# Performance work log

Measured on AMD Instinct MI355X. Metric: run time of the kernel, lower is better.

Reference implementation:

```python
import jax, jax.numpy as jnp
import numpy as np

B, L, N, D = 16, 4096, 512, 256
EPS = 1e-8  # torch F.cosine_similarity default eps


def setup_inputs() -> dict:
    key = jax.random.key(0)
    k1, k2, k3 = jax.random.split(key, 3)
    spk_decoder_out = jax.random.normal(k1, (B, L, D), dtype=jnp.float32)
    profile = jax.random.normal(k2, (B, N, D), dtype=jnp.float32)
    # lengths in [1, N] so every batch has at least one valid profile
    profile_lens = jax.random.randint(k3, (B,), 1, N + 1, dtype=jnp.int32)
    return {"spk_decoder_out": spk_decoder_out, "profile": profile,
            "profile_lens": profile_lens}


def reference(spk_decoder_out, profile, profile_lens):
    # cosine similarity between (B,L,1,D) and (B,1,N,D) along D, computed
    # without materializing the (B,L,N,D) broadcast intermediate
    dots = jnp.einsum('bld,bnd->bln', spk_decoder_out, profile)      # (B,L,N)
    x_norm = jnp.sqrt(jnp.sum(spk_decoder_out * spk_decoder_out, axis=-1))  # (B,L)
    p_norm = jnp.sqrt(jnp.sum(profile * profile, axis=-1))           # (B,N)
    denom = jnp.maximum(x_norm[:, :, None] * p_norm[:, None, :], EPS)
    sim = dots / denom                                               # (B,L,N)

    # pad mask over profiles: True where n >= profile_lens[b]
    n = profile.shape[1]
    mask = jnp.arange(n, dtype=profile_lens.dtype)[None, :] >= profile_lens[:, None]  # (B,N)
    min_value = jnp.finfo(jnp.float32).min
    sim = jnp.where(mask[:, None, :], min_value, sim)
    weights = jax.nn.softmax(sim, axis=-1)
    weights = jnp.where(mask[:, None, :], 0.0, weights)              # (B,L,N)

    spk_embedding = jnp.einsum('bln,bnd->bld', weights, profile)     # (B,L,D)
    return spk_embedding, weights
```

## Files before the change

### kernel.cpp

```cpp
#include <hip/hip_runtime.h>
#include <hip/hip_bf16.h>
#include <math.h>

#define BB 16
#define LL 4096
#define NN 512
#define DD 256

typedef __attribute__((ext_vector_type(8))) short  bf16x8;
typedef __attribute__((ext_vector_type(4))) float  f32x4;
typedef __attribute__((ext_vector_type(4))) unsigned short u16x4;

typedef __attribute__((address_space(1))) const void  gvoid_t;
typedef __attribute__((address_space(3))) void        lvoid_t;

#define GLL16(src, dst) __builtin_amdgcn_global_load_lds((gvoid_t*)(src), (lvoid_t*)(dst), 16, 0, 0)

__device__ __forceinline__ unsigned short f2bf(float x) {
    union { float f; unsigned u; } v; v.f = x;
    unsigned r = v.u + 0x7fffu + ((v.u >> 16) & 1u);
    return (unsigned short)(r >> 16);
}
__device__ __forceinline__ float bfhi(unsigned u) { return __uint_as_float(u & 0xffff0000u); }
__device__ __forceinline__ float bflo(unsigned u) { return __uint_as_float(u << 16); }

__global__ __launch_bounds__(256) void cda_prep(
    const float* __restrict__ P, char* __restrict__ pnI, char* __restrict__ peI)
{
    const int gw   = blockIdx.x * 4 + (threadIdx.x >> 6);
    const int lane = threadIdx.x & 63;
    const float4 v = *(const float4*)(P + (size_t)gw * DD + lane * 4);
    float ss = v.x * v.x + v.y * v.y + v.z * v.z + v.w * v.w;
    #pragma unroll
    for (int off = 32; off > 0; off >>= 1) ss += __shfl_xor(ss, off);
    const float rinv = 1.0f / sqrtf(ss);
    const int n  = gw & (NN - 1);
    const int nl = n & 31;
    const size_t tile = ((size_t)((gw >> 9) * 16 + (n >> 5))) << 14;

    u16x4 h;
    h.x = f2bf(v.x * rinv); h.y = f2bf(v.y * rinv);
    h.z = f2bf(v.z * rinv); h.w = f2bf(v.w * rinv);
    *(u16x4*)(pnI + tile + ((nl * 512 + lane * 8) ^ ((nl & 7) << 4))) = h;

    const int ks = ((nl >> 2) & 3) * 8 + ((nl >> 4) << 2) + (nl & 3);
    const float raw[4] = {v.x, v.y, v.z, v.w};
    #pragma unroll
    for (int j = 0; j < 4; ++j) {
        const int d = lane * 4 + j;
        *(unsigned short*)(peI + tile + ((d * 64 + ks * 2) ^ ((d & 15) << 4))) = f2bf(raw[j]);
    }
}

struct __align__(16) Smem {
    char pn[2][16384];
    union {
        char xstage[32768];
        char pe[2][16384];
    } u;
    float tbl[64];
};

__global__ __launch_bounds__(256, 2) void cda_main(
    const float* __restrict__ X, const char* __restrict__ pnI,
    const char* __restrict__ peI, const int* __restrict__ lens,
    float* __restrict__ out)
{
    __shared__ Smem sm;

    const int id = blockIdx.x;
    const int b  = (id & 7) * 2 + (id >> 9);
    const int l0 = ((id >> 3) & 63) * 64;

    const int tid  = threadIdx.x;
    const int w    = tid >> 6;
    const int lane = tid & 63;
    const int lo   = lane & 15;
    const int g    = lane >> 4;
    const int len  = lens[b];

    const float* Xb  = X + ((size_t)b * LL + l0) * DD;
    const char*  pnB = pnI + (size_t)b * 262144;
    const char*  peB = peI + (size_t)b * 262144;

    #pragma unroll
    for (int q = 0; q < 4; ++q)
        GLL16(pnB + q * 4096 + tid * 16, (char*)sm.pn[0] + q * 4096 + tid * 16);

    #pragma unroll
    for (int rr = 0; rr < 16; ++rr) {
        const int row = w * 16 + rr;
        const float4 v = *(const float4*)(Xb + row * DD + lane * 4);
        float ss = v.x * v.x + v.y * v.y + v.z * v.z + v.w * v.w;
        #pragma unroll
        for (int off = 32; off > 0; off >>= 1) ss += __shfl_xor(ss, off);
        const float inv = 1.0f / sqrtf(ss);
        u16x4 h;
        h.x = f2bf(v.x * inv); h.y = f2bf(v.y * inv);
        h.z = f2bf(v.z * inv); h.w = f2bf(v.w * inv);
        *(u16x4*)(sm.u.xstage + ((row * 512 + lane * 8) ^ ((row & 7) << 4))) = h;
    }
    __syncthreads();
    bf16x8 xf[8];
    #pragma unroll
    for (int ks = 0; ks < 8; ++ks)
        xf[ks] = *(const bf16x8*)(sm.u.xstage +
            (((w * 16 + lo) * 512 + ks * 64 + g * 16) ^ ((lo & 7) << 4)));
    __syncthreads();

    #pragma unroll
    for (int q = 0; q < 4; ++q)
        GLL16(peB + q * 4096 + tid * 16, (char*)sm.u.pe[0] + q * 4096 + tid * 16);

    unsigned pm[16][4];
    float ssum = 0.f;

    #pragma unroll
    for (int c = 0; c < 16; ++c) {
        asm volatile("s_waitcnt vmcnt(0)" ::: "memory");
        __builtin_amdgcn_s_barrier();
        __builtin_amdgcn_sched_barrier(0);
        if (c < 15) {
            const char* src = pnB + (c + 1) * 16384;
            char* dst = (char*)sm.pn[(c + 1) & 1];
            #pragma unroll
            for (int q = 0; q < 4; ++q)
                GLL16(src + q * 4096 + tid * 16, dst + q * 4096 + tid * 16);
        }
        const char* pnL = (const char*)sm.pn[c & 1];
        f32x4 a0 = (f32x4){0.f, 0.f, 0.f, 0.f};
        f32x4 a1 = (f32x4){0.f, 0.f, 0.f, 0.f};
        #pragma unroll
        for (int ks = 0; ks < 8; ++ks) {
            const bf16x8 f0 = *(const bf16x8*)(pnL +
                ((lo * 512 + ks * 64 + g * 16) ^ ((lo & 7) << 4)));
            a0 = __builtin_amdgcn_mfma_f32_16x16x32_bf16(f0, xf[ks], a0, 0, 0, 0);
            const bf16x8 f1 = *(const bf16x8*)(pnL +
                (((16 + lo) * 512 + ks * 64 + g * 16) ^ ((lo & 7) << 4)));
            a1 = __builtin_amdgcn_mfma_f32_16x16x32_bf16(f1, xf[ks], a1, 0, 0, 0);
        }
        unsigned short pw[8];
        #pragma unroll
        for (int r = 0; r < 4; ++r) {
            const int n0 = c * 32 + g * 4 + r;
            const float p0 = (n0 < len) ? __expf(a0[r]) : 0.f;
            ssum += p0; pw[r] = f2bf(p0);
            const float p1 = (n0 + 16 < len) ? __expf(a1[r]) : 0.f;
            ssum += p1; pw[4 + r] = f2bf(p1);
        }
        pm[c][0] = (unsigned)pw[0] | ((unsigned)pw[1] << 16);
        pm[c][1] = (unsigned)pw[2] | ((unsigned)pw[3] << 16);
        pm[c][2] = (unsigned)pw[4] | ((unsigned)pw[5] << 16);
        pm[c][3] = (unsigned)pw[6] | ((unsigned)pw[7] << 16);
    }

    ssum += __shfl_xor(ssum, 16);
    ssum += __shfl_xor(ssum, 32);
    const float sinv = 1.0f / ssum;
    if (g == 0) sm.tbl[w * 16 + lo] = sinv;

    f32x4 e[16];
    #pragma unroll
    for (int i = 0; i < 16; ++i) e[i] = (f32x4){0.f, 0.f, 0.f, 0.f};

    float* Wrow = out + (size_t)BB * LL * DD
                + ((size_t)b * LL + l0 + w * 16 + lo) * (size_t)NN;

    #pragma unroll
    for (int c = 0; c < 16; ++c) {
        if (c == 0) asm volatile("s_waitcnt vmcnt(0)" ::: "memory");
        else        asm volatile("s_waitcnt vmcnt(2)" ::: "memory");
        __builtin_amdgcn_s_barrier();
        __builtin_amdgcn_sched_barrier(0);
        if (c < 15) {
            const char* src = peB + (c + 1) * 16384;
            char* dst = (char*)sm.u.pe[(c + 1) & 1];
            #pragma unroll
            for (int q = 0; q < 4; ++q)
                GLL16(src + q * 4096 + tid * 16, dst + q * 4096 + tid * 16);
        }
        float4 v0, v1;
        v0.x = bflo(pm[c][0]) * sinv; v0.y = bfhi(pm[c][0]) * sinv;
        v0.z = bflo(pm[c][1]) * sinv; v0.w = bfhi(pm[c][1]) * sinv;
        v1.x = bflo(pm[c][2]) * sinv; v1.y = bfhi(pm[c][2]) * sinv;
        v1.z = bflo(pm[c][3]) * sinv; v1.w = bfhi(pm[c][3]) * sinv;
        *(float4*)(Wrow + c * 32 + g * 4)      = v0;
        *(float4*)(Wrow + c * 32 + 16 + g * 4) = v1;

        union { unsigned u[4]; bf16x8 v; } pf;
        pf.u[0] = pm[c][0]; pf.u[1] = pm[c][1];
        pf.u[2] = pm[c][2]; pf.u[3] = pm[c][3];
        const char* peL = (const char*)sm.u.pe[c & 1];
        #pragma unroll
        for (int df = 0; df < 16; ++df) {
            const bf16x8 bf = *(const bf16x8*)(peL +
                (((df * 16 + lo) * 64 + g * 16) ^ (lo << 4)));
            e[df] = __builtin_amdgcn_mfma_f32_16x16x32_bf16(pf.v, bf, e[df], 0, 0, 0);
        }
    }

    float t4[4];
    #pragma unroll
    for (int r = 0; r < 4; ++r) t4[r] = sm.tbl[w * 16 + g * 4 + r];
    char* scr = (char*)sm.pn + w * 8192;
    float* Eout = out + ((size_t)b * LL + l0 + w * 16) * DD;
    #pragma unroll
    for (int r = 0; r < 4; ++r) {
        #pragma unroll
        for (int df = 0; df < 16; ++df)
            *(float*)(scr + g * 1040 + (size_t)(df * 16 + lo) * 4) = e[df][r] * t4[r];
        #pragma unroll
        for (int it = 0; it < 4; ++it) {
            const float4 t = *(const float4*)(scr + it * 1040 + lane * 16);
            *(float4*)(Eout + (size_t)(it * 4 + r) * DD + lane * 4) = t;
        }
    }
}

extern "C" void kernel_launch(void* const* d_in, const int* in_sizes, int n_in,
                              void* d_out, int out_size, void* d_ws, size_t ws_size,
                              hipStream_t stream) {
    const float* X    = (const float*)d_in[0];
    const float* P    = (const float*)d_in[1];
    const int*   lens = (const int*)d_in[2];
    float*       out  = (float*)d_out;

    char* pnI = (char*)d_ws;
    char* peI = (char*)d_ws + 4194304;

    hipLaunchKernelGGL(cda_prep, dim3(BB * NN / 4), dim3(256), 0, stream, P, pnI, peI);
    hipLaunchKernelGGL(cda_main, dim3(1024), dim3(256), 0, stream, X, pnI, peI, lens, out);
}
```

Measured before the change: 96.40 us.

## Pre-swizzle profile tiles into MFMA fragment order and cut LDS to raise occupancy

The prep kernel now processes a whole 32-row tile per block and writes the normalized and raw profile tiles already arranged in MFMA fragment order, using LDS for the transpose of the pe layout. This makes the main kernel's LDS reads linear per lane, with no XOR swizzle. The main kernel drops the per-row normalization of X before bf16 conversion and instead scales the logits by the row's inverse norm. It reuses shared buffers so LDS shrinks to 48KB, which allows launch bounds of 3 blocks per CU, and the pe prefetch moves into the last pn iteration. In exchange there is more register pressure, a slight precision change from rounding unnormalized X to bf16, and less overlap of the first pe load.

```diff
diff --git a/kernel.cpp b/kernel.cpp
--- a/kernel.cpp
+++ b/kernel.cpp
@@ -10,6 +10,7 @@
 typedef __attribute__((ext_vector_type(8))) short  bf16x8;
 typedef __attribute__((ext_vector_type(4))) float  f32x4;
 typedef __attribute__((ext_vector_type(4))) unsigned short u16x4;
+typedef __attribute__((ext_vector_type(8))) unsigned short u16x8;
 
 typedef __attribute__((address_space(1))) const void  gvoid_t;
 typedef __attribute__((address_space(3))) void        lvoid_t;
@@ -27,46 +28,73 @@
 __global__ __launch_bounds__(256) void cda_prep(
     const float* __restrict__ P, char* __restrict__ pnI, char* __restrict__ peI)
 {
-    const int gw   = blockIdx.x * 4 + (threadIdx.x >> 6);
-    const int lane = threadIdx.x & 63;
-    const float4 v = *(const float4*)(P + (size_t)gw * DD + lane * 4);
-    float ss = v.x * v.x + v.y * v.y + v.z * v.z + v.w * v.w;
-    #pragma unroll
-    for (int off = 32; off > 0; off >>= 1) ss += __shfl_xor(ss, off);
+    __shared__ __align__(16) char raw[16384];
+
+    const int blk = blockIdx.x;
+    const int b   = blk >> 4;
+    const int c   = blk & 15;
+    const int tid = threadIdx.x;
+    const int nl  = tid >> 3;
+    const int sub = tid & 7;
+
+    const float* rowp = P + (((size_t)b * NN + c * 32 + nl) * DD + sub * 32);
+    float4 v[8];
+    #pragma unroll
+    for (int k = 0; k < 8; ++k) v[k] = *(const float4*)(rowp + k * 4);
+
+    float ss = 0.f;
+    #pragma unroll
+    for (int k = 0; k < 8; ++k)
+        ss += v[k].x * v[k].x + v[k].y * v[k].y + v[k].z * v[k].z + v[k].w * v[k].w;
+    ss += __shfl_xor(ss, 1); ss += __shfl_xor(ss, 2); ss += __shfl_xor(ss, 4);
     const float rinv = 1.0f / sqrtf(ss);
-    const int n  = gw & (NN - 1);
-    const int nl = n & 31;
-    const size_t tile = ((size_t)((gw >> 9) * 16 + (n >> 5))) << 14;
-
-    u16x4 h;
-    h.x = f2bf(v.x * rinv); h.y = f2bf(v.y * rinv);
-    h.z = f2bf(v.z * rinv); h.w = f2bf(v.w * rinv);
-    *(u16x4*)(pnI + tile + ((nl * 512 + lane * 8) ^ ((nl & 7) << 4))) = h;
-
-    const int ks = ((nl >> 2) & 3) * 8 + ((nl >> 4) << 2) + (nl & 3);
-    const float raw[4] = {v.x, v.y, v.z, v.w};
-    #pragma unroll
-    for (int j = 0; j < 4; ++j) {
-        const int d = lane * 4 + j;
-        *(unsigned short*)(peI + tile + ((d * 64 + ks * 2) ^ ((d & 15) << 4))) = f2bf(raw[j]);
-    }
-}
-
-struct __align__(16) Smem {
-    char pn[2][16384];
-    union {
-        char xstage[32768];
-        char pe[2][16384];
-    } u;
-    float tbl[64];
-};
-
-__global__ __launch_bounds__(256, 2) void cda_main(
+
+    const size_t tile = ((size_t)b * 16 + c) * 16384;
+
+    #pragma unroll
+    for (int g = 0; g < 4; ++g) {
+        u16x8 h;
+        #pragma unroll
+        for (int j = 0; j < 8; ++j) {
+            const int dl = g * 8 + j;
+            const float f = ((const float*)&v[dl >> 2])[dl & 3];
+            h[j] = f2bf(f * rinv);
+        }
+        *(u16x8*)(pnI + tile + sub * 2048 + (nl >> 4) * 1024 + (g * 16 + (nl & 15)) * 16) = h;
+    }
+
+    #pragma unroll
+    for (int g = 0; g < 4; ++g) {
+        u16x8 h;
+        #pragma unroll
+        for (int j = 0; j < 8; ++j) {
+            const int dl = g * 8 + j;
+            h[j] = f2bf(((const float*)&v[dl >> 2])[dl & 3]);
+        }
+        *(u16x8*)(raw + ((nl * 512 + sub * 64 + g * 16) ^ ((nl & 7) << 4))) = h;
+    }
+    __syncthreads();
+
+    unsigned short arr[32];
+    #pragma unroll
+    for (int r = 0; r < 32; ++r)
+        arr[r] = *(const unsigned short*)(raw + ((r * 512 + tid * 2) ^ ((r & 7) << 4)));
+    #pragma unroll
+    for (int g = 0; g < 4; ++g) {
+        u16x8 h;
+        #pragma unroll
+        for (int j = 0; j < 8; ++j)
+            h[j] = arr[g * 4 + (j & 3) + 16 * (j >> 2)];
+        *(u16x8*)(peI + tile + (tid >> 4) * 1024 + (g * 16 + (tid & 15)) * 16) = h;
+    }
+}
+
+__global__ __launch_bounds__(256, 3) void cda_main(
     const float* __restrict__ X, const char* __restrict__ pnI,
     const char* __restrict__ peI, const int* __restrict__ lens,
     float* __restrict__ out)
 {
-    __shared__ Smem sm;
+    __shared__ __align__(16) char sm[49152];
 
     const int id = blockIdx.x;
     const int b  = (id & 7) * 2 + (id >> 9);
@@ -85,8 +113,9 @@
 
     #pragma unroll
     for (int q = 0; q < 4; ++q)
-        GLL16(pnB + q * 4096 + tid * 16, (char*)sm.pn[0] + q * 4096 + tid * 16);
-
+        GLL16(pnB + q * 4096 + tid * 16, sm + q * 4096 + tid * 16);
+
+    float xinv = 0.f;
     #pragma unroll
     for (int rr = 0; rr < 16; ++rr) {
         const int row = w * 16 + rr;
@@ -95,22 +124,16 @@
         #pragma unroll
         for (int off = 32; off > 0; off >>= 1) ss += __shfl_xor(ss, off);
         const float inv = 1.0f / sqrtf(ss);
-        u16x4 h;
-        h.x = f2bf(v.x * inv); h.y = f2bf(v.y * inv);
-        h.z = f2bf(v.z * inv); h.w = f2bf(v.w * inv);
-        *(u16x4*)(sm.u.xstage + ((row * 512 + lane * 8) ^ ((row & 7) << 4))) = h;
-    }
-    __syncthreads();
+        if (rr == lo) xinv = inv;
+        u16x4 h; h.x = f2bf(v.x); h.y = f2bf(v.y); h.z = f2bf(v.z); h.w = f2bf(v.w);
+        *(u16x4*)(sm + 16384 + ((row * 512 + lane * 8) ^ ((row & 7) << 4))) = h;
+    }
     bf16x8 xf[8];
     #pragma unroll
     for (int ks = 0; ks < 8; ++ks)
-        xf[ks] = *(const bf16x8*)(sm.u.xstage +
+        xf[ks] = *(const bf16x8*)(sm + 16384 +
             (((w * 16 + lo) * 512 + ks * 64 + g * 16) ^ ((lo & 7) << 4)));
     __syncthreads();
-
-    #pragma unroll
-    for (int q = 0; q < 4; ++q)
-        GLL16(peB + q * 4096 + tid * 16, (char*)sm.u.pe[0] + q * 4096 + tid * 16);
 
     unsigned pm[16][4];
     float ssum = 0.f;
@@ -122,30 +145,32 @@
         __builtin_amdgcn_sched_barrier(0);
         if (c < 15) {
             const char* src = pnB + (c + 1) * 16384;
-            char* dst = (char*)sm.pn[(c + 1) & 1];
+            char* dst = sm + ((c + 1) & 1) * 16384;
             #pragma unroll
             for (int q = 0; q < 4; ++q)
                 GLL16(src + q * 4096 + tid * 16, dst + q * 4096 + tid * 16);
-        }
-        const char* pnL = (const char*)sm.pn[c & 1];
+        } else {
+            #pragma unroll
+            for (int q = 0; q < 4; ++q)
+                GLL16(peB + q * 4096 + tid * 16, sm + q * 4096 + tid * 16);
+        }
+        const char* pnL = sm + (c & 1) * 16384;
         f32x4 a0 = (f32x4){0.f, 0.f, 0.f, 0.f};
         f32x4 a1 = (f32x4){0.f, 0.f, 0.f, 0.f};
         #pragma unroll
         for (int ks = 0; ks < 8; ++ks) {
-            const bf16x8 f0 = *(const bf16x8*)(pnL +
-                ((lo * 512 + ks * 64 + g * 16) ^ ((lo & 7) << 4)));
+            const bf16x8 f0 = *(const bf16x8*)(pnL + ks * 2048 + lane * 16);
+            const bf16x8 f1 = *(const bf16x8*)(pnL + ks * 2048 + 1024 + lane * 16);
             a0 = __builtin_amdgcn_mfma_f32_16x16x32_bf16(f0, xf[ks], a0, 0, 0, 0);
-            const bf16x8 f1 = *(const bf16x8*)(pnL +
-                (((16 + lo) * 512 + ks * 64 + g * 16) ^ ((lo & 7) << 4)));
             a1 = __builtin_amdgcn_mfma_f32_16x16x32_bf16(f1, xf[ks], a1, 0, 0, 0);
         }
         unsigned short pw[8];
         #pragma unroll
         for (int r = 0; r < 4; ++r) {
             const int n0 = c * 32 + g * 4 + r;
-            const float p0 = (n0 < len) ? __expf(a0[r]) : 0.f;
+            const float p0 = (n0 < len) ? __expf(a0[r] * xinv) : 0.f;
             ssum += p0; pw[r] = f2bf(p0);
-            const float p1 = (n0 + 16 < len) ? __expf(a1[r]) : 0.f;
+            const float p1 = (n0 + 16 < len) ? __expf(a1[r] * xinv) : 0.f;
             ssum += p1; pw[4 + r] = f2bf(p1);
         }
         pm[c][0] = (unsigned)pw[0] | ((unsigned)pw[1] << 16);
@@ -157,7 +182,6 @@
     ssum += __shfl_xor(ssum, 16);
     ssum += __shfl_xor(ssum, 32);
     const float sinv = 1.0f / ssum;
-    if (g == 0) sm.tbl[w * 16 + lo] = sinv;
 
     f32x4 e[16];
     #pragma unroll
@@ -174,7 +198,7 @@
         __builtin_amdgcn_sched_barrier(0);
         if (c < 15) {
             const char* src = peB + (c + 1) * 16384;
-            char* dst = (char*)sm.u.pe[(c + 1) & 1];
+            char* dst = sm + ((c + 1) & 1) * 16384;
             #pragma unroll
             for (int q = 0; q < 4; ++q)
                 GLL16(src + q * 4096 + tid * 16, dst + q * 4096 + tid * 16);
@@ -190,28 +214,27 @@
         union { unsigned u[4]; bf16x8 v; } pf;
         pf.u[0] = pm[c][0]; pf.u[1] = pm[c][1];
         pf.u[2] = pm[c][2]; pf.u[3] = pm[c][3];
-        const char* peL = (const char*)sm.u.pe[c & 1];
+        const char* peL = sm + (c & 1) * 16384;
         #pragma unroll
         for (int df = 0; df < 16; ++df) {
-            const bf16x8 bf = *(const bf16x8*)(peL +
-                (((df * 16 + lo) * 64 + g * 16) ^ (lo << 4)));
+            const bf16x8 bf = *(const bf16x8*)(peL + df * 1024 + lane * 16);
             e[df] = __builtin_amdgcn_mfma_f32_16x16x32_bf16(pf.v, bf, e[df], 0, 0, 0);
         }
     }
 
     float t4[4];
     #pragma unroll
-    for (int r = 0; r < 4; ++r) t4[r] = sm.tbl[w * 16 + g * 4 + r];
-    char* scr = (char*)sm.pn + w * 8192;
+    for (int r = 0; r < 4; ++r) t4[r] = __shfl(sinv, g * 4 + r);
+    char* scr = sm + 32768 + w * 4096;
     float* Eout = out + ((size_t)b * LL + l0 + w * 16) * DD;
     #pragma unroll
     for (int r = 0; r < 4; ++r) {
         #pragma unroll
         for (int df = 0; df < 16; ++df)
-            *(float*)(scr + g * 1040 + (size_t)(df * 16 + lo) * 4) = e[df][r] * t4[r];
+            *(float*)(scr + g * 1024 + df * 64 + lo * 4) = e[df][r] * t4[r];
         #pragma unroll
         for (int it = 0; it < 4; ++it) {
-            const float4 t = *(const float4*)(scr + it * 1040 + lane * 16);
+            const float4 t = *(const float4*)(scr + it * 1024 + lane * 16);
             *(float4*)(Eout + (size_t)(it * 4 + r) * DD + lane * 4) = t;
         }
     }
@@ -228,6 +251,6 @@
     char* pnI = (char*)d_ws;
     char* peI = (char*)d_ws + 4194304;
 
-    hipLaunchKernelGGL(cda_prep, dim3(BB * NN / 4), dim3(256), 0, stream, P, pnI, peI);
+    hipLaunchKernelGGL(cda_prep, dim3(BB * 16), dim3(256), 0, stream, P, pnI, peI);
     hipLaunchKernelGGL(cda_main, dim3(1024), dim3(256), 0, stream, X, pnI, peI, lens, out);
 }
```

New measurement: 112.6 us. 16.8% more time.
